# Optimization experiments

Measured on AMD Instinct MI355X. Metric: run time of the kernel, lower is better.

## Reference

```python
import jax, jax.numpy as jnp
import numpy as np

N = 50000      # nodes (single 'Node' ntype, dataset 'B')
R = 3          # number of edge types
E = 600000     # edges per etype
D = 128        # in_feats = hid_feats = emb_feats, num_heads = 1
L = 3          # hconv layers = n_layers + 1
EPS = 1e-5     # BatchNorm eps
SLOPE = 0.2    # GATConv leaky_relu negative_slope


def setup_inputs() -> dict:
    key = jax.random.key(0)
    ks = jax.random.split(key, 7)
    x = jax.random.normal(ks[0], (N, D), dtype=jnp.float32)
    src = jax.random.randint(ks[1], (R, E), 0, N, dtype=jnp.int32)
    dst = jax.random.randint(ks[2], (R, E), 0, N, dtype=jnp.int32)
    # Stacked per-layer, per-etype GATConv params (scaled for sane magnitudes)
    Ws = jax.random.normal(ks[3], (L, R, D, D), dtype=jnp.float32) * (1.0 / np.sqrt(D).astype(np.float32))
    attn_l = jax.random.normal(ks[4], (L, R, D), dtype=jnp.float32) * 0.05
    attn_r = jax.random.normal(ks[5], (L, R, D), dtype=jnp.float32) * 0.05
    bias = jax.random.normal(ks[6], (L, R, D), dtype=jnp.float32) * 0.05
    gamma = jnp.ones((L, D), dtype=jnp.float32)
    beta = jnp.zeros((L, D), dtype=jnp.float32)
    return {"x": x, "src": src, "dst": dst, "Ws": Ws, "attn_l": attn_l,
            "attn_r": attn_r, "bias": bias, "gamma": gamma, "beta": beta}


def _gat(h, s, d, W, al, ar, b):
    """DGL GATConv (num_heads=1, residual=Identity since in==out): returns pre-activation output."""
    z = h @ W                                   # [N, D] projected features
    el = (z * al).sum(-1)                       # [N] src attention logits
    er = (z * ar).sum(-1)                       # [N] dst attention logits
    e = el[s] + er[d]                           # [E]
    e = jnp.where(e > 0, e, SLOPE * e)          # leaky_relu
    # edge softmax over incoming edges of each dst node (numerically stable)
    m = jax.ops.segment_max(e, d, num_segments=N)
    m = jnp.where(jnp.isfinite(m), m, 0.0)      # empty segments -> 0
    ex = jnp.exp(e - m[d])
    ssum = jax.ops.segment_sum(ex, d, num_segments=N)
    alpha = ex / ssum[d]                        # [E]
    agg = jax.ops.segment_sum(alpha[:, None] * z[s], d, num_segments=N)  # [N, D]
    return agg + h + b                          # scatter-sum + identity residual + bias


def _bn(x, g, b):
    # Training-mode BatchNorm1d: batch stats, biased variance
    mu = x.mean(0)
    var = x.var(0)
    return (x - mu) * jax.lax.rsqrt(var + EPS) * g + b


def reference(x, src, dst, Ws, attn_l, attn_r, bias, gamma, beta):
    h = x
    for i in range(L):
        # per-etype GATConv, vmapped over the R relation types
        outs = jax.vmap(_gat, in_axes=(None, 0, 0, 0, 0, 0, 0))(
            h, src, dst, Ws[i], attn_l[i], attn_r[i], bias[i])  # [R, N, D]
        if i < L - 1:
            outs = jax.nn.relu(outs)            # activation inside GATConv (not on last layer)
        h = outs.sum(0)                         # HeteroGraphConv aggregate='sum'
        h = _bn(h, gamma[i], beta[i])           # self.norms[i]
    return h
```

## Files before the change

kernel.cpp:

```cpp
#include <hip/hip_runtime.h>
#include <math.h>

#define N_NODES 50000
#define R_ETYPES 3
#define E_EDGES 600000
#define D_FEAT 128
#define L_LAYERS 3
#define BN_EPS 1e-5f
#define LR_SLOPE 0.2f

#define XCD_SPLIT 8
#define DST_RANGE ((N_NODES + XCD_SPLIT - 1) / XCD_SPLIT)
#define EPT 16
#define CHUNK_E (256 * EPT)

#define SCAN_ELEMS 2048
#define SCAN_NBLK ((N_NODES + SCAN_ELEMS - 1) / SCAN_ELEMS)
#define RP_STRIDE 50008

typedef unsigned short ushortT;
typedef short bf16x8 __attribute__((ext_vector_type(8)));
typedef float f32x4 __attribute__((ext_vector_type(4)));

__device__ __forceinline__ float bf2f(ushortT u) {
    return __uint_as_float(((unsigned int)u) << 16);
}
__device__ __forceinline__ ushortT f2bf(float f) {
    unsigned int u = __float_as_uint(f);
    u += 0x7fffu + ((u >> 16) & 1u);
    return (ushortT)(u >> 16);
}

__global__ __launch_bounds__(256) void hist_kernel(const int* __restrict__ dst,
                                                   int* __restrict__ deg) {
    int range = blockIdx.x & (XCD_SPLIT - 1);
    int chunk = blockIdx.x >> 3;
    int lo = range * DST_RANGE;
    int hi = lo + DST_RANGE; if (hi > N_NODES) hi = N_NODES;
    int base = chunk * CHUNK_E;
#pragma unroll
    for (int it = 0; it < EPT; it++) {
        int i = base + it * 256 + threadIdx.x;
        if (i < R_ETYPES * E_EDGES) {
            int d = dst[i];
            if (d >= lo && d < hi) {
                int r = i / E_EDGES;
                atomicAdd(&deg[r * N_NODES + d], 1);
            }
        }
    }
}

__global__ __launch_bounds__(256) void scan1_kernel(const int* __restrict__ deg,
                                                    int* __restrict__ row_ptr,
                                                    int* __restrict__ bsum) {
    int bx = blockIdx.x;
    int r = bx / SCAN_NBLK;
    int b = bx % SCAN_NBLK;
    int t = threadIdx.x;
    const int* dg = deg + r * N_NODES;
    int* rp = row_ptr + r * RP_STRIDE;
    int idx0 = b * SCAN_ELEMS + t * 8;

    int e[8];
    if (idx0 + 7 < N_NODES) {
        int4 v0 = *(const int4*)(dg + idx0);
        int4 v1 = *(const int4*)(dg + idx0 + 4);
        e[0] = v0.x; e[1] = v0.y; e[2] = v0.z; e[3] = v0.w;
        e[4] = v1.x; e[5] = v1.y; e[6] = v1.z; e[7] = v1.w;
    } else {
#pragma unroll
        for (int j = 0; j < 8; j++) e[j] = (idx0 + j < N_NODES) ? dg[idx0 + j] : 0;
    }
    int pre[8];
    int s = 0;
#pragma unroll
    for (int j = 0; j < 8; j++) { pre[j] = s; s += e[j]; }

    __shared__ int lds[256];
    lds[t] = s;
    __syncthreads();
    for (int off = 1; off < 256; off <<= 1) {
        int vv = (t >= off) ? lds[t - off] : 0;
        __syncthreads();
        lds[t] += vv;
        __syncthreads();
    }
    int tpre = lds[t] - s;
    if (t == 255) bsum[bx] = lds[255];

    if (idx0 + 7 < N_NODES) {
        int4 o0 = make_int4(tpre + pre[0], tpre + pre[1], tpre + pre[2], tpre + pre[3]);
        int4 o1 = make_int4(tpre + pre[4], tpre + pre[5], tpre + pre[6], tpre + pre[7]);
        *(int4*)(rp + idx0) = o0;
        *(int4*)(rp + idx0 + 4) = o1;
    } else {
#pragma unroll
        for (int j = 0; j < 8; j++)
            if (idx0 + j < N_NODES) rp[idx0 + j] = tpre + pre[j];
    }
}

__global__ __launch_bounds__(64) void scan2_kernel(int* __restrict__ bsum) {
    int r = blockIdx.x;
    int lane = threadIdx.x;
    int own = (lane < SCAN_NBLK) ? bsum[r * SCAN_NBLK + lane] : 0;
    int v = own;
    for (int off = 1; off < 32; off <<= 1) {
        int u = __shfl_up(v, off);
        if (lane >= off) v += u;
    }
    if (lane < SCAN_NBLK) bsum[r * SCAN_NBLK + lane] = v - own;
}

__global__ __launch_bounds__(256) void scan3_kernel(int* __restrict__ row_ptr,
                                                    int* __restrict__ cursor,
                                                    const int* __restrict__ bsum) {
    int bx = blockIdx.x;
    int r = bx / SCAN_NBLK;
    int b = bx % SCAN_NBLK;
    int t = threadIdx.x;
    int off = bsum[r * SCAN_NBLK + b];
    int* rp = row_ptr + r * RP_STRIDE;
    int* cur = cursor + r * N_NODES;
    int idx0 = b * SCAN_ELEMS + t * 8;
    if (b == 0 && t == 0) rp[N_NODES] = E_EDGES;
    if (idx0 + 7 < N_NODES) {
        int4 v0 = *(const int4*)(rp + idx0);
        int4 v1 = *(const int4*)(rp + idx0 + 4);
        v0.x += off; v0.y += off; v0.z += off; v0.w += off;
        v1.x += off; v1.y += off; v1.z += off; v1.w += off;
        *(int4*)(rp + idx0) = v0;
        *(int4*)(rp + idx0 + 4) = v1;
        *(int4*)(cur + idx0) = v0;
        *(int4*)(cur + idx0 + 4) = v1;
    } else {
#pragma unroll
        for (int j = 0; j < 8; j++)
            if (idx0 + j < N_NODES) {
                int vv = rp[idx0 + j] + off;
                rp[idx0 + j] = vv;
                cur[idx0 + j] = vv;
            }
    }
}

__global__ __launch_bounds__(256) void scatter_kernel(const int* __restrict__ src,
                                                      const int* __restrict__ dst,
                                                      int* __restrict__ cursor,
                                                      int* __restrict__ col) {
    int range = blockIdx.x & (XCD_SPLIT - 1);
    int chunk = blockIdx.x >> 3;
    int lo = range * DST_RANGE;
    int hi = lo + DST_RANGE; if (hi > N_NODES) hi = N_NODES;
    int base = chunk * CHUNK_E;
#pragma unroll
    for (int it = 0; it < EPT; it++) {
        int i = base + it * 256 + threadIdx.x;
        if (i < R_ETYPES * E_EDGES) {
            int d = dst[i];
            if (d >= lo && d < hi) {
                int r = i / E_EDGES;
                int pos = atomicAdd(&cursor[r * N_NODES + d], 1);
                col[(size_t)r * E_EDGES + pos] = src[i];
            }
        }
    }
}

__global__ __launch_bounds__(256) void wt_kernel(const float* __restrict__ Ws,
                                                 ushortT* __restrict__ Wt) {
    int idx = blockIdx.x * 256 + threadIdx.x;
    if (idx >= L_LAYERS * R_ETYPES * D_FEAT * D_FEAT) return;
    int lr = idx >> 14;
    int rem = idx & 16383;
    int n = rem >> 7;
    int k = rem & 127;
    Wt[idx] = f2bf(Ws[lr * 16384 + k * 128 + n]);
}

__global__ __launch_bounds__(256) void h0_kernel(const float* __restrict__ x,
                                                 ushortT* __restrict__ hb) {
    int idx = blockIdx.x * 256 + threadIdx.x;
    if (idx < N_NODES * D_FEAT) hb[idx] = f2bf(x[idx]);
}

__global__ __launch_bounds__(256) void gemm_mfma_kernel(
    const ushortT* __restrict__ hb, const ushortT* __restrict__ Wt_l,
    ushortT* __restrict__ z3, float* __restrict__ el3, float* __restrict__ er3,
    const float* __restrict__ al_l, const float* __restrict__ ar_l) {
    __shared__ short As[16][128][8];
    __shared__ short Bs[16][128][8];
    int tid = threadIdx.x;
    int r = blockIdx.y;
    int row0 = blockIdx.x * 128;
    const ushortT* Wt = Wt_l + (size_t)r * 16384;
    ushortT* z = z3 + (size_t)r * N_NODES * D_FEAT;
    float* el = el3 + (size_t)r * N_NODES;
    float* er = er3 + (size_t)r * N_NODES;
    const float* al = al_l + r * 128;
    const float* ar = ar_l + r * 128;

#pragma unroll
    for (int i = 0; i < 8; i++) {
        int slot = tid + i * 256;
        int g = slot & 15;
        int m = slot >> 4;
        int row = row0 + m;
        bf16x8 av = {};
        if (row < N_NODES) av = *(const bf16x8*)(hb + (size_t)row * 128 + g * 8);
        *(bf16x8*)&As[g][m][0] = av;
        *(bf16x8*)&Bs[g][m][0] = *(const bf16x8*)(Wt + m * 128 + g * 8);
    }
    __syncthreads();

    int wave = tid >> 6;
    int lane = tid & 63;
    int quad = lane >> 4;
    int cl = lane & 15;

    f32x4 acc[2][8];
#pragma unroll
    for (int mf = 0; mf < 2; mf++)
#pragma unroll
        for (int nb = 0; nb < 8; nb++) acc[mf][nb] = (f32x4){0.f, 0.f, 0.f, 0.f};

#pragma unroll
    for (int kk = 0; kk < 4; kk++) {
        int g = kk * 4 + quad;
        bf16x8 af[2], bfr[8];
#pragma unroll
        for (int mf = 0; mf < 2; mf++)
            af[mf] = *(const bf16x8*)&As[g][wave * 32 + mf * 16 + cl][0];
#pragma unroll
        for (int nb = 0; nb < 8; nb++)
            bfr[nb] = *(const bf16x8*)&Bs[g][nb * 16 + cl][0];
#pragma unroll
        for (int mf = 0; mf < 2; mf++)
#pragma unroll
            for (int nb = 0; nb < 8; nb++)
                acc[mf][nb] = __builtin_amdgcn_mfma_f32_16x16x32_bf16(
                    af[mf], bfr[nb], acc[mf][nb], 0, 0, 0);
    }

    float alv[8], arv[8];
#pragma unroll
    for (int nb = 0; nb < 8; nb++) {
        alv[nb] = al[nb * 16 + cl];
        arv[nb] = ar[nb * 16 + cl];
    }
#pragma unroll
    for (int mf = 0; mf < 2; mf++) {
        float elp[4] = {0.f, 0.f, 0.f, 0.f}, erp[4] = {0.f, 0.f, 0.f, 0.f};
#pragma unroll
        for (int nb = 0; nb < 8; nb++) {
#pragma unroll
            for (int reg = 0; reg < 4; reg++) {
                float zv = acc[mf][nb][reg];
                elp[reg] += zv * alv[nb];
                erp[reg] += zv * arv[nb];
            }
        }
#pragma unroll
        for (int mask = 1; mask < 16; mask <<= 1) {
#pragma unroll
            for (int reg = 0; reg < 4; reg++) {
                elp[reg] += __shfl_xor(elp[reg], mask);
                erp[reg] += __shfl_xor(erp[reg], mask);
            }
        }
#pragma unroll
        for (int reg = 0; reg < 4; reg++) {
            int row = row0 + wave * 32 + mf * 16 + quad * 4 + reg;
            if (row < N_NODES) {
#pragma unroll
                for (int nb = 0; nb < 8; nb++)
                    z[(size_t)row * 128 + nb * 16 + cl] = f2bf(acc[mf][nb][reg]);
                if (cl == 0) { el[row] = elp[reg]; er[row] = erp[reg]; }
            }
        }
    }
}

__global__ __launch_bounds__(256) void agg3_kernel(
    const ushortT* __restrict__ z3, const float* __restrict__ el3,
    const float* __restrict__ er3, const ushortT* __restrict__ hb,
    const float* __restrict__ bias_l, const int* __restrict__ col,
    const int* __restrict__ row_ptr, float* __restrict__ h_next, int do_relu) {
    int lane = threadIdx.x & 63;
    int v = blockIdx.x * 4 + (threadIdx.x >> 6);
    const size_t ND = (size_t)N_NODES * D_FEAT;

    ushort2 hraw = *(const ushort2*)(hb + (size_t)v * 128 + lane * 2);
    float h0 = bf2f(hraw.x), h1 = bf2f(hraw.y);
    float t0 = 0.f, t1 = 0.f;
#pragma unroll
    for (int r = 0; r < R_ETYPES; r++) {
        const ushortT* z = z3 + (size_t)r * ND;
        const float* el = el3 + (size_t)r * N_NODES;
        const int* cc = col + (size_t)r * E_EDGES;
        const int* rp = row_ptr + (size_t)r * RP_STRIDE;
        int beg = rp[v], end = rp[v + 1];
        float er_v = er3[(size_t)r * N_NODES + v];

        float ss0 = 0.f, ss1 = 0.f, ss2 = 0.f, ss3 = 0.f;
        float a00 = 0.f, a01 = 0.f, a02 = 0.f, a03 = 0.f;
        float a10 = 0.f, a11 = 0.f, a12 = 0.f, a13 = 0.f;
        int p = beg;
        for (; p + 4 <= end; p += 4) {
            int s0 = cc[p], s1 = cc[p + 1], s2 = cc[p + 2], s3 = cc[p + 3];
            float e0 = el[s0] + er_v, e1 = el[s1] + er_v;
            float e2 = el[s2] + er_v, e3 = el[s3] + er_v;
            e0 = fmaxf(e0, 0.f) + LR_SLOPE * fminf(e0, 0.f);
            e1 = fmaxf(e1, 0.f) + LR_SLOPE * fminf(e1, 0.f);
            e2 = fmaxf(e2, 0.f) + LR_SLOPE * fminf(e2, 0.f);
            e3 = fmaxf(e3, 0.f) + LR_SLOPE * fminf(e3, 0.f);
            float x0 = __expf(e0), x1 = __expf(e1);
            float x2 = __expf(e2), x3 = __expf(e3);
            ushort2 zz0 = *(const ushort2*)(z + (size_t)s0 * 128 + lane * 2);
            ushort2 zz1 = *(const ushort2*)(z + (size_t)s1 * 128 + lane * 2);
            ushort2 zz2 = *(const ushort2*)(z + (size_t)s2 * 128 + lane * 2);
            ushort2 zz3 = *(const ushort2*)(z + (size_t)s3 * 128 + lane * 2);
            ss0 += x0; ss1 += x1; ss2 += x2; ss3 += x3;
            a00 = fmaf(x0, bf2f(zz0.x), a00); a10 = fmaf(x0, bf2f(zz0.y), a10);
            a01 = fmaf(x1, bf2f(zz1.x), a01); a11 = fmaf(x1, bf2f(zz1.y), a11);
            a02 = fmaf(x2, bf2f(zz2.x), a02); a12 = fmaf(x2, bf2f(zz2.y), a12);
            a03 = fmaf(x3, bf2f(zz3.x), a03); a13 = fmaf(x3, bf2f(zz3.y), a13);
        }
        for (; p < end; p++) {
            int s = cc[p];
            float e = el[s] + er_v;
            e = fmaxf(e, 0.f) + LR_SLOPE * fminf(e, 0.f);
            float ex = __expf(e);
            ushort2 zz = *(const ushort2*)(z + (size_t)s * 128 + lane * 2);
            ss0 += ex;
            a00 = fmaf(ex, bf2f(zz.x), a00);
            a10 = fmaf(ex, bf2f(zz.y), a10);
        }
        float ssum = (ss0 + ss1) + (ss2 + ss3);
        float a0 = (a00 + a01) + (a02 + a03);
        float a1 = (a10 + a11) + (a12 + a13);
        float inv = (end > beg) ? 1.f / ssum : 0.f;
        float v0 = a0 * inv + h0 + bias_l[r * 128 + lane * 2];
        float v1 = a1 * inv + h1 + bias_l[r * 128 + lane * 2 + 1];
        if (do_relu) { v0 = fmaxf(v0, 0.f); v1 = fmaxf(v1, 0.f); }
        t0 += v0; t1 += v1;
    }
    *(float2*)(h_next + (size_t)v * 128 + lane * 2) = make_float2(t0, t1);
}

__global__ __launch_bounds__(128) void bn_stats_kernel(const float* __restrict__ x,
                                                       float* __restrict__ stats) {
    int t = threadIdx.x;
    float s = 0.f, q = 0.f;
    for (int v = blockIdx.x; v < N_NODES; v += gridDim.x) {
        float xv = x[(size_t)v * 128 + t];
        s += xv;
        q += xv * xv;
    }
    atomicAdd(&stats[t], s);
    atomicAdd(&stats[128 + t], q);
}

__global__ __launch_bounds__(256) void hprep_kernel(const float* __restrict__ x,
                                                    const float* __restrict__ stats,
                                                    const float* __restrict__ g,
                                                    const float* __restrict__ b,
                                                    ushortT* __restrict__ hb) {
    int idx = blockIdx.x * 256 + threadIdx.x;
    if (idx >= N_NODES * D_FEAT) return;
    int c = idx & 127;
    const float invN = 1.0f / (float)N_NODES;
    float mu = stats[c] * invN;
    float var = stats[128 + c] * invN - mu * mu;
    float sc = g[c] * rsqrtf(var + BN_EPS);
    hb[idx] = f2bf((x[idx] - mu) * sc + b[c]);
}

__global__ __launch_bounds__(256) void bn_apply_kernel(const float* __restrict__ x,
                                                       const float* __restrict__ stats,
                                                       const float* __restrict__ g,
                                                       const float* __restrict__ b,
                                                       float* __restrict__ out) {
    int idx = blockIdx.x * 256 + threadIdx.x;
    if (idx >= N_NODES * D_FEAT) return;
    int c = idx & 127;
    const float invN = 1.0f / (float)N_NODES;
    float mu = stats[c] * invN;
    float var = stats[128 + c] * invN - mu * mu;
    out[idx] = (x[idx] - mu) * rsqrtf(var + BN_EPS) * g[c] + b[c];
}

extern "C" void kernel_launch(void* const* d_in, const int* in_sizes, int n_in,
                              void* d_out, int out_size, void* d_ws, size_t ws_size,
                              hipStream_t stream) {
    const float* x      = (const float*)d_in[0];
    const int*   src    = (const int*)d_in[1];
    const int*   dst    = (const int*)d_in[2];
    const float* Ws     = (const float*)d_in[3];
    const float* attn_l = (const float*)d_in[4];
    const float* attn_r = (const float*)d_in[5];
    const float* bias   = (const float*)d_in[6];
    const float* gamma  = (const float*)d_in[7];
    const float* beta   = (const float*)d_in[8];

    const size_t ND = (size_t)N_NODES * D_FEAT;
    const int total_e = R_ETYPES * E_EDGES;

    ushortT* z3 = (ushortT*)d_ws;
    ushortT* hb = z3 + 3 * ND;
    ushortT* Wt = hb + ND;
    float* h_next = (float*)(Wt + 9 * 16384);
    float* el3   = h_next + ND;
    float* er3   = el3 + 3 * N_NODES;
    float* stats = er3 + 3 * N_NODES;
    int* deg     = (int*)(stats + 3 * 256);
    int* row_ptr = deg + 3 * N_NODES;
    int* cursor  = row_ptr + 3 * RP_STRIDE;
    int* col     = cursor + 3 * N_NODES;
    int* bsum    = col + (size_t)total_e;
    size_t needed = (char*)(bsum + 3 * SCAN_NBLK) - (char*)d_ws;
    if (ws_size < needed) return;

    wt_kernel<<<(L_LAYERS * R_ETYPES * 16384 + 255) / 256, 256, 0, stream>>>(Ws, Wt);
    h0_kernel<<<(int)((ND + 255) / 256), 256, 0, stream>>>(x, hb);

    (void)hipMemsetAsync(deg, 0, (size_t)3 * N_NODES * sizeof(int), stream);
    (void)hipMemsetAsync(stats, 0, 3 * 256 * sizeof(float), stream);
    {
        const int csr_chunks = (total_e + CHUNK_E - 1) / CHUNK_E;
        hist_kernel<<<csr_chunks * XCD_SPLIT, 256, 0, stream>>>(dst, deg);
        scan1_kernel<<<R_ETYPES * SCAN_NBLK, 256, 0, stream>>>(deg, row_ptr, bsum);
        scan2_kernel<<<R_ETYPES, 64, 0, stream>>>(bsum);
        scan3_kernel<<<R_ETYPES * SCAN_NBLK, 256, 0, stream>>>(row_ptr, cursor, bsum);
        scatter_kernel<<<csr_chunks * XCD_SPLIT, 256, 0, stream>>>(src, dst, cursor, col);
    }

    for (int l = 0; l < L_LAYERS; l++) {
        gemm_mfma_kernel<<<dim3((N_NODES + 127) / 128, R_ETYPES), 256, 0, stream>>>(
            hb, Wt + (size_t)l * R_ETYPES * 16384, z3, el3, er3,
            attn_l + (size_t)l * R_ETYPES * 128, attn_r + (size_t)l * R_ETYPES * 128);
        agg3_kernel<<<(N_NODES + 3) / 4, 256, 0, stream>>>(
            z3, el3, er3, hb, bias + (size_t)l * R_ETYPES * 128,
            col, row_ptr, h_next, (l < L_LAYERS - 1) ? 1 : 0);
        float* st = stats + l * 256;
        bn_stats_kernel<<<512, 128, 0, stream>>>(h_next, st);
        if (l < L_LAYERS - 1) {
            hprep_kernel<<<(int)((ND + 255) / 256), 256, 0, stream>>>(
                h_next, st, gamma + (size_t)l * D_FEAT, beta + (size_t)l * D_FEAT, hb);
        } else {
            bn_apply_kernel<<<(int)((ND + 255) / 256), 256, 0, stream>>>(
                h_next, st, gamma + (size_t)l * D_FEAT, beta + (size_t)l * D_FEAT,
                (float*)d_out);
        }
    }
}
```

Before: 771.1 us.

## Precompute edge weights and aggregate 4 nodes per wave with 16-byte gathers

Adds a separate pass that computes exp(leaky_relu(el[src]+er[dst])) per edge into a buffer, using a new row_of array written by the scatter kernel. The aggregation kernel now processes four destination nodes per wave, with 16 lanes each loading 8 bf16 features as a uint4, and loops to the maximum degree among the four with masked lanes. BN statistics use float4 loads with a shared-memory reduction. This reduces per-edge dependent latency and widens the gathers, at the cost of extra edge-array traffic, an extra launch per layer, and divergence when degrees differ.

```diff
diff --git a/kernel.cpp b/kernel.cpp
--- a/kernel.cpp
+++ b/kernel.cpp
@@ -24,6 +24,12 @@
 
 __device__ __forceinline__ float bf2f(ushortT u) {
     return __uint_as_float(((unsigned int)u) << 16);
+}
+__device__ __forceinline__ float bf2f_lo(unsigned int d) {
+    return __uint_as_float(d << 16);
+}
+__device__ __forceinline__ float bf2f_hi(unsigned int d) {
+    return __uint_as_float(d & 0xffff0000u);
 }
 __device__ __forceinline__ ushortT f2bf(float f) {
     unsigned int u = __float_as_uint(f);
@@ -148,7 +154,8 @@
 __global__ __launch_bounds__(256) void scatter_kernel(const int* __restrict__ src,
                                                       const int* __restrict__ dst,
                                                       int* __restrict__ cursor,
-                                                      int* __restrict__ col) {
+                                                      int* __restrict__ col,
+                                                      int* __restrict__ row_of) {
     int range = blockIdx.x & (XCD_SPLIT - 1);
     int chunk = blockIdx.x >> 3;
     int lo = range * DST_RANGE;
@@ -163,6 +170,7 @@
                 int r = i / E_EDGES;
                 int pos = atomicAdd(&cursor[r * N_NODES + d], 1);
                 col[(size_t)r * E_EDGES + pos] = src[i];
+                row_of[(size_t)r * E_EDGES + pos] = d;
             }
         }
     }
@@ -282,84 +290,134 @@
     }
 }
 
-__global__ __launch_bounds__(256) void agg3_kernel(
-    const ushortT* __restrict__ z3, const float* __restrict__ el3,
-    const float* __restrict__ er3, const ushortT* __restrict__ hb,
-    const float* __restrict__ bias_l, const int* __restrict__ col,
-    const int* __restrict__ row_ptr, float* __restrict__ h_next, int do_relu) {
-    int lane = threadIdx.x & 63;
-    int v = blockIdx.x * 4 + (threadIdx.x >> 6);
-    const size_t ND = (size_t)N_NODES * D_FEAT;
-
-    ushort2 hraw = *(const ushort2*)(hb + (size_t)v * 128 + lane * 2);
-    float h0 = bf2f(hraw.x), h1 = bf2f(hraw.y);
-    float t0 = 0.f, t1 = 0.f;
+__global__ __launch_bounds__(256) void edge_w_kernel(const int* __restrict__ col,
+                                                     const int* __restrict__ row_of,
+                                                     const float* __restrict__ el3,
+                                                     const float* __restrict__ er3,
+                                                     float* __restrict__ wv) {
+    int r = blockIdx.y;
+    const int* cc = col + (size_t)r * E_EDGES;
+    const int* ro = row_of + (size_t)r * E_EDGES;
+    const float* el = el3 + (size_t)r * N_NODES;
+    const float* er = er3 + (size_t)r * N_NODES;
+    float* w = wv + (size_t)r * E_EDGES;
+    int base = blockIdx.x * 2048;
+#pragma unroll
+    for (int i = 0; i < 8; i++) {
+        int p = base + i * 256 + threadIdx.x;
+        if (p < E_EDGES) {
+            float e = el[cc[p]] + er[ro[p]];
+            e = fmaxf(e, 0.f) + LR_SLOPE * fminf(e, 0.f);
+            w[p] = __expf(e);
+        }
+    }
+}
+
+__global__ __launch_bounds__(256) void agg5_kernel(
+    const ushortT* __restrict__ z3, const ushortT* __restrict__ hb,
+    const float* __restrict__ wv, const int* __restrict__ col,
+    const int* __restrict__ row_ptr, const float* __restrict__ bias_l,
+    float* __restrict__ h_next, int do_relu) {
+    int tid = threadIdx.x;
+    int lane = tid & 63;
+    int g = lane >> 4;
+    int f = lane & 15;
+    int v = blockIdx.x * 16 + (tid >> 6) * 4 + g;
+
+    uint4 hv = *(const uint4*)(hb + (size_t)v * 128 + f * 8);
+    float h[8];
+    h[0] = bf2f_lo(hv.x); h[1] = bf2f_hi(hv.x);
+    h[2] = bf2f_lo(hv.y); h[3] = bf2f_hi(hv.y);
+    h[4] = bf2f_lo(hv.z); h[5] = bf2f_hi(hv.z);
+    h[6] = bf2f_lo(hv.w); h[7] = bf2f_hi(hv.w);
+
+    float total[8];
+#pragma unroll
+    for (int j = 0; j < 8; j++) total[j] = 0.f;
+
 #pragma unroll
     for (int r = 0; r < R_ETYPES; r++) {
-        const ushortT* z = z3 + (size_t)r * ND;
-        const float* el = el3 + (size_t)r * N_NODES;
+        const int* rp = row_ptr + (size_t)r * RP_STRIDE;
+        int beg = rp[v];
+        int deg = rp[v + 1] - beg;
+        int m = deg;
+        m = max(m, __shfl_xor(m, 16));
+        m = max(m, __shfl_xor(m, 32));
+        int maxdeg = __builtin_amdgcn_readfirstlane(m);
+
         const int* cc = col + (size_t)r * E_EDGES;
-        const int* rp = row_ptr + (size_t)r * RP_STRIDE;
-        int beg = rp[v], end = rp[v + 1];
-        float er_v = er3[(size_t)r * N_NODES + v];
-
-        float ss0 = 0.f, ss1 = 0.f, ss2 = 0.f, ss3 = 0.f;
-        float a00 = 0.f, a01 = 0.f, a02 = 0.f, a03 = 0.f;
-        float a10 = 0.f, a11 = 0.f, a12 = 0.f, a13 = 0.f;
-        int p = beg;
-        for (; p + 4 <= end; p += 4) {
-            int s0 = cc[p], s1 = cc[p + 1], s2 = cc[p + 2], s3 = cc[p + 3];
-            float e0 = el[s0] + er_v, e1 = el[s1] + er_v;
-            float e2 = el[s2] + er_v, e3 = el[s3] + er_v;
-            e0 = fmaxf(e0, 0.f) + LR_SLOPE * fminf(e0, 0.f);
-            e1 = fmaxf(e1, 0.f) + LR_SLOPE * fminf(e1, 0.f);
-            e2 = fmaxf(e2, 0.f) + LR_SLOPE * fminf(e2, 0.f);
-            e3 = fmaxf(e3, 0.f) + LR_SLOPE * fminf(e3, 0.f);
-            float x0 = __expf(e0), x1 = __expf(e1);
-            float x2 = __expf(e2), x3 = __expf(e3);
-            ushort2 zz0 = *(const ushort2*)(z + (size_t)s0 * 128 + lane * 2);
-            ushort2 zz1 = *(const ushort2*)(z + (size_t)s1 * 128 + lane * 2);
-            ushort2 zz2 = *(const ushort2*)(z + (size_t)s2 * 128 + lane * 2);
-            ushort2 zz3 = *(const ushort2*)(z + (size_t)s3 * 128 + lane * 2);
-            ss0 += x0; ss1 += x1; ss2 += x2; ss3 += x3;
-            a00 = fmaf(x0, bf2f(zz0.x), a00); a10 = fmaf(x0, bf2f(zz0.y), a10);
-            a01 = fmaf(x1, bf2f(zz1.x), a01); a11 = fmaf(x1, bf2f(zz1.y), a11);
-            a02 = fmaf(x2, bf2f(zz2.x), a02); a12 = fmaf(x2, bf2f(zz2.y), a12);
-            a03 = fmaf(x3, bf2f(zz3.x), a03); a13 = fmaf(x3, bf2f(zz3.y), a13);
-        }
-        for (; p < end; p++) {
+        const float* w = wv + (size_t)r * E_EDGES;
+        const ushortT* zr = z3 + (size_t)r * N_NODES * D_FEAT;
+
+        float acc[8];
+#pragma unroll
+        for (int j = 0; j < 8; j++) acc[j] = 0.f;
+        float ssum = 0.f;
+
+        for (int it = 0; it < maxdeg; it++) {
+            int p = min(beg + it, E_EDGES - 1);
+            bool valid = it < deg;
             int s = cc[p];
-            float e = el[s] + er_v;
-            e = fmaxf(e, 0.f) + LR_SLOPE * fminf(e, 0.f);
-            float ex = __expf(e);
-            ushort2 zz = *(const ushort2*)(z + (size_t)s * 128 + lane * 2);
-            ss0 += ex;
-            a00 = fmaf(ex, bf2f(zz.x), a00);
-            a10 = fmaf(ex, bf2f(zz.y), a10);
-        }
-        float ssum = (ss0 + ss1) + (ss2 + ss3);
-        float a0 = (a00 + a01) + (a02 + a03);
-        float a1 = (a10 + a11) + (a12 + a13);
-        float inv = (end > beg) ? 1.f / ssum : 0.f;
-        float v0 = a0 * inv + h0 + bias_l[r * 128 + lane * 2];
-        float v1 = a1 * inv + h1 + bias_l[r * 128 + lane * 2 + 1];
-        if (do_relu) { v0 = fmaxf(v0, 0.f); v1 = fmaxf(v1, 0.f); }
-        t0 += v0; t1 += v1;
-    }
-    *(float2*)(h_next + (size_t)v * 128 + lane * 2) = make_float2(t0, t1);
-}
-
-__global__ __launch_bounds__(128) void bn_stats_kernel(const float* __restrict__ x,
-                                                       float* __restrict__ stats) {
+            float wt = w[p];
+            wt = valid ? wt : 0.f;
+            s = valid ? s : 0;
+            uint4 zz = *(const uint4*)(zr + (size_t)s * 128 + f * 8);
+            ssum += wt;
+            acc[0] = fmaf(wt, bf2f_lo(zz.x), acc[0]);
+            acc[1] = fmaf(wt, bf2f_hi(zz.x), acc[1]);
+            acc[2] = fmaf(wt, bf2f_lo(zz.y), acc[2]);
+            acc[3] = fmaf(wt, bf2f_hi(zz.y), acc[3]);
+            acc[4] = fmaf(wt, bf2f_lo(zz.z), acc[4]);
+            acc[5] = fmaf(wt, bf2f_hi(zz.z), acc[5]);
+            acc[6] = fmaf(wt, bf2f_lo(zz.w), acc[6]);
+            acc[7] = fmaf(wt, bf2f_hi(zz.w), acc[7]);
+        }
+        float inv = (deg > 0) ? 1.f / ssum : 0.f;
+        float4 b0 = *(const float4*)(bias_l + r * 128 + f * 8);
+        float4 b1 = *(const float4*)(bias_l + r * 128 + f * 8 + 4);
+        float bb[8] = {b0.x, b0.y, b0.z, b0.w, b1.x, b1.y, b1.z, b1.w};
+#pragma unroll
+        for (int j = 0; j < 8; j++) {
+            float val = fmaf(acc[j], inv, h[j]) + bb[j];
+            if (do_relu) val = fmaxf(val, 0.f);
+            total[j] += val;
+        }
+    }
+    float* outp = h_next + (size_t)v * 128 + f * 8;
+    *(float4*)(outp) = make_float4(total[0], total[1], total[2], total[3]);
+    *(float4*)(outp + 4) = make_float4(total[4], total[5], total[6], total[7]);
+}
+
+__global__ __launch_bounds__(256) void bn_stats2_kernel(const float* __restrict__ x,
+                                                        float* __restrict__ stats) {
     int t = threadIdx.x;
-    float s = 0.f, q = 0.f;
-    for (int v = blockIdx.x; v < N_NODES; v += gridDim.x) {
-        float xv = x[(size_t)v * 128 + t];
-        s += xv;
-        q += xv * xv;
-    }
-    atomicAdd(&stats[t], s);
-    atomicAdd(&stats[128 + t], q);
+    int cg = (t & 31) * 4;
+    int rl = t >> 5;
+    float4 s = make_float4(0.f, 0.f, 0.f, 0.f);
+    float4 q = make_float4(0.f, 0.f, 0.f, 0.f);
+    for (int v = blockIdx.x * 8 + rl; v < N_NODES; v += 8 * gridDim.x) {
+        float4 xv = *(const float4*)(x + (size_t)v * 128 + cg);
+        s.x += xv.x; s.y += xv.y; s.z += xv.z; s.w += xv.w;
+        q.x += xv.x * xv.x; q.y += xv.y * xv.y;
+        q.z += xv.z * xv.z; q.w += xv.w * xv.w;
+    }
+    __shared__ float ls[8][32][8];
+    ls[rl][t & 31][0] = s.x; ls[rl][t & 31][1] = s.y;
+    ls[rl][t & 31][2] = s.z; ls[rl][t & 31][3] = s.w;
+    ls[rl][t & 31][4] = q.x; ls[rl][t & 31][5] = q.y;
+    ls[rl][t & 31][6] = q.z; ls[rl][t & 31][7] = q.w;
+    __syncthreads();
+    if (rl == 0) {
+        int c = t & 31;
+#pragma unroll
+        for (int j = 0; j < 4; j++) {
+            float sv = 0.f, qv = 0.f;
+#pragma unroll
+            for (int k = 0; k < 8; k++) { sv += ls[k][c][j]; qv += ls[k][c][4 + j]; }
+            atomicAdd(&stats[cg + j], sv);
+            atomicAdd(&stats[128 + cg + j], qv);
+        }
+    }
 }
 
 __global__ __launch_bounds__(256) void hprep_kernel(const float* __restrict__ x,
@@ -413,12 +471,14 @@
     float* h_next = (float*)(Wt + 9 * 16384);
     float* el3   = h_next + ND;
     float* er3   = el3 + 3 * N_NODES;
-    float* stats = er3 + 3 * N_NODES;
+    float* wv    = er3 + 3 * N_NODES;
+    float* stats = wv + (size_t)total_e;
     int* deg     = (int*)(stats + 3 * 256);
     int* row_ptr = deg + 3 * N_NODES;
     int* cursor  = row_ptr + 3 * RP_STRIDE;
     int* col     = cursor + 3 * N_NODES;
-    int* bsum    = col + (size_t)total_e;
+    int* row_of  = col + (size_t)total_e;
+    int* bsum    = row_of + (size_t)total_e;
     size_t needed = (char*)(bsum + 3 * SCAN_NBLK) - (char*)d_ws;
     if (ws_size < needed) return;
 
@@ -433,18 +493,22 @@
         scan1_kernel<<<R_ETYPES * SCAN_NBLK, 256, 0, stream>>>(deg, row_ptr, bsum);
         scan2_kernel<<<R_ETYPES, 64, 0, stream>>>(bsum);
         scan3_kernel<<<R_ETYPES * SCAN_NBLK, 256, 0, stream>>>(row_ptr, cursor, bsum);
-        scatter_kernel<<<csr_chunks * XCD_SPLIT, 256, 0, stream>>>(src, dst, cursor, col);
-    }
-
+        scatter_kernel<<<csr_chunks * XCD_SPLIT, 256, 0, stream>>>(src, dst, cursor,
+                                                                   col, row_of);
+    }
+
+    const int ew_grid = (E_EDGES + 2047) / 2048;
     for (int l = 0; l < L_LAYERS; l++) {
         gemm_mfma_kernel<<<dim3((N_NODES + 127) / 128, R_ETYPES), 256, 0, stream>>>(
             hb, Wt + (size_t)l * R_ETYPES * 16384, z3, el3, er3,
             attn_l + (size_t)l * R_ETYPES * 128, attn_r + (size_t)l * R_ETYPES * 128);
-        agg3_kernel<<<(N_NODES + 3) / 4, 256, 0, stream>>>(
-            z3, el3, er3, hb, bias + (size_t)l * R_ETYPES * 128,
-            col, row_ptr, h_next, (l < L_LAYERS - 1) ? 1 : 0);
+        edge_w_kernel<<<dim3(ew_grid, R_ETYPES), 256, 0, stream>>>(
+            col, row_of, el3, er3, wv);
+        agg5_kernel<<<N_NODES / 16, 256, 0, stream>>>(
+            z3, hb, wv, col, row_ptr, bias + (size_t)l * R_ETYPES * 128,
+            h_next, (l < L_LAYERS - 1) ? 1 : 0);
         float* st = stats + l * 256;
-        bn_stats_kernel<<<512, 128, 0, stream>>>(h_next, st);
+        bn_stats2_kernel<<<1024, 256, 0, stream>>>(h_next, st);
         if (l < L_LAYERS - 1) {
             hprep_kernel<<<(int)((ND + 255) / 256), 256, 0, stream>>>(
                 h_next, st, gamma + (size_t)l * D_FEAT, beta + (size_t)l * D_FEAT, hb);
```

New measurement: 979.2 us. +27.0%, slower.

## Precompute per-edge attention weights in separate kernel; vectorize BN stats reduction

Applied to the files above, without the earlier changes.

Adds a row_of array in the CSR scatter and a new edge_w_kernel that computes exp(leaky_relu(el[src]+er[dst])) once per edge, so the aggregation kernel no longer does the redundant per-lane el gathers and exp. In the old kernel every one of the 64 lanes in a wave recomputed the same weight. The BN stats kernel is also rewritten to use float4 loads and a shared-memory reduction with fewer blocks and atomics. The cost is an extra kernel launch per layer plus extra global traffic for writing and reading the weight and row_of arrays.

```diff
diff --git a/kernel.cpp b/kernel.cpp
--- a/kernel.cpp
+++ b/kernel.cpp
@@ -148,7 +148,8 @@
 __global__ __launch_bounds__(256) void scatter_kernel(const int* __restrict__ src,
                                                       const int* __restrict__ dst,
                                                       int* __restrict__ cursor,
-                                                      int* __restrict__ col) {
+                                                      int* __restrict__ col,
+                                                      int* __restrict__ row_of) {
     int range = blockIdx.x & (XCD_SPLIT - 1);
     int chunk = blockIdx.x >> 3;
     int lo = range * DST_RANGE;
@@ -163,6 +164,7 @@
                 int r = i / E_EDGES;
                 int pos = atomicAdd(&cursor[r * N_NODES + d], 1);
                 col[(size_t)r * E_EDGES + pos] = src[i];
+                row_of[(size_t)r * E_EDGES + pos] = d;
             }
         }
     }
@@ -282,11 +284,34 @@
     }
 }
 
-__global__ __launch_bounds__(256) void agg3_kernel(
-    const ushortT* __restrict__ z3, const float* __restrict__ el3,
-    const float* __restrict__ er3, const ushortT* __restrict__ hb,
-    const float* __restrict__ bias_l, const int* __restrict__ col,
-    const int* __restrict__ row_ptr, float* __restrict__ h_next, int do_relu) {
+__global__ __launch_bounds__(256) void edge_w_kernel(const int* __restrict__ col,
+                                                     const int* __restrict__ row_of,
+                                                     const float* __restrict__ el3,
+                                                     const float* __restrict__ er3,
+                                                     float* __restrict__ wv) {
+    int r = blockIdx.y;
+    const int* cc = col + (size_t)r * E_EDGES;
+    const int* ro = row_of + (size_t)r * E_EDGES;
+    const float* el = el3 + (size_t)r * N_NODES;
+    const float* er = er3 + (size_t)r * N_NODES;
+    float* w = wv + (size_t)r * E_EDGES;
+    int base = blockIdx.x * 2048;
+#pragma unroll
+    for (int i = 0; i < 8; i++) {
+        int p = base + i * 256 + threadIdx.x;
+        if (p < E_EDGES) {
+            float e = el[cc[p]] + er[ro[p]];
+            e = fmaxf(e, 0.f) + LR_SLOPE * fminf(e, 0.f);
+            w[p] = __expf(e);
+        }
+    }
+}
+
+__global__ __launch_bounds__(256) void agg4_kernel(
+    const ushortT* __restrict__ z3, const ushortT* __restrict__ hb,
+    const float* __restrict__ wv, const int* __restrict__ col,
+    const int* __restrict__ row_ptr, const float* __restrict__ bias_l,
+    float* __restrict__ h_next, int do_relu) {
     int lane = threadIdx.x & 63;
     int v = blockIdx.x * 4 + (threadIdx.x >> 6);
     const size_t ND = (size_t)N_NODES * D_FEAT;
@@ -297,11 +322,10 @@
 #pragma unroll
     for (int r = 0; r < R_ETYPES; r++) {
         const ushortT* z = z3 + (size_t)r * ND;
-        const float* el = el3 + (size_t)r * N_NODES;
         const int* cc = col + (size_t)r * E_EDGES;
+        const float* w = wv + (size_t)r * E_EDGES;
         const int* rp = row_ptr + (size_t)r * RP_STRIDE;
         int beg = rp[v], end = rp[v + 1];
-        float er_v = er3[(size_t)r * N_NODES + v];
 
         float ss0 = 0.f, ss1 = 0.f, ss2 = 0.f, ss3 = 0.f;
         float a00 = 0.f, a01 = 0.f, a02 = 0.f, a03 = 0.f;
@@ -309,14 +333,7 @@
         int p = beg;
         for (; p + 4 <= end; p += 4) {
             int s0 = cc[p], s1 = cc[p + 1], s2 = cc[p + 2], s3 = cc[p + 3];
-            float e0 = el[s0] + er_v, e1 = el[s1] + er_v;
-            float e2 = el[s2] + er_v, e3 = el[s3] + er_v;
-            e0 = fmaxf(e0, 0.f) + LR_SLOPE * fminf(e0, 0.f);
-            e1 = fmaxf(e1, 0.f) + LR_SLOPE * fminf(e1, 0.f);
-            e2 = fmaxf(e2, 0.f) + LR_SLOPE * fminf(e2, 0.f);
-            e3 = fmaxf(e3, 0.f) + LR_SLOPE * fminf(e3, 0.f);
-            float x0 = __expf(e0), x1 = __expf(e1);
-            float x2 = __expf(e2), x3 = __expf(e3);
+            float x0 = w[p], x1 = w[p + 1], x2 = w[p + 2], x3 = w[p + 3];
             ushort2 zz0 = *(const ushort2*)(z + (size_t)s0 * 128 + lane * 2);
             ushort2 zz1 = *(const ushort2*)(z + (size_t)s1 * 128 + lane * 2);
             ushort2 zz2 = *(const ushort2*)(z + (size_t)s2 * 128 + lane * 2);
@@ -329,9 +346,7 @@
         }
         for (; p < end; p++) {
             int s = cc[p];
-            float e = el[s] + er_v;
-            e = fmaxf(e, 0.f) + LR_SLOPE * fminf(e, 0.f);
-            float ex = __expf(e);
+            float ex = w[p];
             ushort2 zz = *(const ushort2*)(z + (size_t)s * 128 + lane * 2);
             ss0 += ex;
             a00 = fmaf(ex, bf2f(zz.x), a00);
@@ -349,17 +364,36 @@
     *(float2*)(h_next + (size_t)v * 128 + lane * 2) = make_float2(t0, t1);
 }
 
-__global__ __launch_bounds__(128) void bn_stats_kernel(const float* __restrict__ x,
-                                                       float* __restrict__ stats) {
+__global__ __launch_bounds__(256) void bn_stats3_kernel(const float* __restrict__ x,
+                                                        float* __restrict__ stats) {
     int t = threadIdx.x;
-    float s = 0.f, q = 0.f;
-    for (int v = blockIdx.x; v < N_NODES; v += gridDim.x) {
-        float xv = x[(size_t)v * 128 + t];
-        s += xv;
-        q += xv * xv;
-    }
-    atomicAdd(&stats[t], s);
-    atomicAdd(&stats[128 + t], q);
+    int cg = (t & 31) * 4;
+    int rl = t >> 5;
+    float4 s = make_float4(0.f, 0.f, 0.f, 0.f);
+    float4 q = make_float4(0.f, 0.f, 0.f, 0.f);
+    for (int v = blockIdx.x * 8 + rl; v < N_NODES; v += 8 * gridDim.x) {
+        float4 xv = *(const float4*)(x + (size_t)v * 128 + cg);
+        s.x += xv.x; s.y += xv.y; s.z += xv.z; s.w += xv.w;
+        q.x += xv.x * xv.x; q.y += xv.y * xv.y;
+        q.z += xv.z * xv.z; q.w += xv.w * xv.w;
+    }
+    __shared__ float ls[8][32][9];
+    ls[rl][t & 31][0] = s.x; ls[rl][t & 31][1] = s.y;
+    ls[rl][t & 31][2] = s.z; ls[rl][t & 31][3] = s.w;
+    ls[rl][t & 31][4] = q.x; ls[rl][t & 31][5] = q.y;
+    ls[rl][t & 31][6] = q.z; ls[rl][t & 31][7] = q.w;
+    __syncthreads();
+    if (rl == 0) {
+        int c = t & 31;
+#pragma unroll
+        for (int j = 0; j < 4; j++) {
+            float sv = 0.f, qv = 0.f;
+#pragma unroll
+            for (int k = 0; k < 8; k++) { sv += ls[k][c][j]; qv += ls[k][c][4 + j]; }
+            atomicAdd(&stats[cg + j], sv);
+            atomicAdd(&stats[128 + cg + j], qv);
+        }
+    }
 }
 
 __global__ __launch_bounds__(256) void hprep_kernel(const float* __restrict__ x,
@@ -413,12 +447,14 @@
     float* h_next = (float*)(Wt + 9 * 16384);
     float* el3   = h_next + ND;
     float* er3   = el3 + 3 * N_NODES;
-    float* stats = er3 + 3 * N_NODES;
+    float* wv    = er3 + 3 * N_NODES;
+    float* stats = wv + (size_t)total_e;
     int* deg     = (int*)(stats + 3 * 256);
     int* row_ptr = deg + 3 * N_NODES;
     int* cursor  = row_ptr + 3 * RP_STRIDE;
     int* col     = cursor + 3 * N_NODES;
-    int* bsum    = col + (size_t)total_e;
+    int* row_of  = col + (size_t)total_e;
+    int* bsum    = row_of + (size_t)total_e;
     size_t needed = (char*)(bsum + 3 * SCAN_NBLK) - (char*)d_ws;
     if (ws_size < needed) return;
 
@@ -433,18 +469,22 @@
         scan1_kernel<<<R_ETYPES * SCAN_NBLK, 256, 0, stream>>>(deg, row_ptr, bsum);
         scan2_kernel<<<R_ETYPES, 64, 0, stream>>>(bsum);
         scan3_kernel<<<R_ETYPES * SCAN_NBLK, 256, 0, stream>>>(row_ptr, cursor, bsum);
-        scatter_kernel<<<csr_chunks * XCD_SPLIT, 256, 0, stream>>>(src, dst, cursor, col);
-    }
-
+        scatter_kernel<<<csr_chunks * XCD_SPLIT, 256, 0, stream>>>(src, dst, cursor,
+                                                                   col, row_of);
+    }
+
+    const int ew_grid = (E_EDGES + 2047) / 2048;
     for (int l = 0; l < L_LAYERS; l++) {
         gemm_mfma_kernel<<<dim3((N_NODES + 127) / 128, R_ETYPES), 256, 0, stream>>>(
             hb, Wt + (size_t)l * R_ETYPES * 16384, z3, el3, er3,
             attn_l + (size_t)l * R_ETYPES * 128, attn_r + (size_t)l * R_ETYPES * 128);
-        agg3_kernel<<<(N_NODES + 3) / 4, 256, 0, stream>>>(
-            z3, el3, er3, hb, bias + (size_t)l * R_ETYPES * 128,
-            col, row_ptr, h_next, (l < L_LAYERS - 1) ? 1 : 0);
+        edge_w_kernel<<<dim3(ew_grid, R_ETYPES), 256, 0, stream>>>(
+            col, row_of, el3, er3, wv);
+        agg4_kernel<<<(N_NODES + 3) / 4, 256, 0, stream>>>(
+            z3, hb, wv, col, row_ptr, bias + (size_t)l * R_ETYPES * 128,
+            h_next, (l < L_LAYERS - 1) ? 1 : 0);
         float* st = stats + l * 256;
-        bn_stats_kernel<<<512, 128, 0, stream>>>(h_next, st);
+        bn_stats3_kernel<<<64, 256, 0, stream>>>(h_next, st);
         if (l < L_LAYERS - 1) {
             hprep_kernel<<<(int)((ND + 255) / 256), 256, 0, stream>>>(
                 h_next, st, gamma + (size_t)l * D_FEAT, beta + (size_t)l * D_FEAT, hb);
```

New measurement: 780.6 us. About the same (+1.2%).
